# Kernel optimization log

Hardware: AMD Instinct MI355X
Metric: run time of the kernel (lower is better)

Reference implementation:

```python
import jax, jax.numpy as jnp
import numpy as np

B, T, C, H = 4, 4096, 1024, 64

def setup_inputs() -> dict:
    key = jax.random.key(0)
    k1, k2, k3, k4 = jax.random.split(key, 4)
    x = jax.random.normal(k1, (B, T, C), dtype=jnp.float32)
    # Linear(n_embed, head_size, bias=False), stored as [in, out] for x @ W
    s = 1.0 / np.sqrt(C)
    Wq = jax.random.uniform(k2, (C, H), dtype=jnp.float32, minval=-s, maxval=s)
    Wk = jax.random.uniform(k3, (C, H), dtype=jnp.float32, minval=-s, maxval=s)
    Wv = jax.random.uniform(k4, (C, H), dtype=jnp.float32, minval=-s, maxval=s)
    return {"x": x, "Wq": Wq, "Wk": Wk, "Wv": Wv}

def reference(x, Wq, Wk, Wv):
    Bn, Tn, Cn = x.shape
    q = x @ Wq  # [B,T,H]
    k = x @ Wk  # [B,T,H]
    v = x @ Wv  # [B,T,H]
    # NOTE: original scales by C**-0.5 (embedding dim), not head_size**-0.5
    wei = jnp.einsum('bqh,bkh->bqk', q, k) * (Cn ** -0.5)  # [B,T,T]
    causal = jnp.tril(jnp.ones((Tn, Tn), dtype=bool))
    wei = jnp.where(causal, wei, -jnp.inf)
    wei = jax.nn.softmax(wei, axis=-1)
    out = jnp.einsum('bqk,bkh->bqh', wei, v)  # [B,T,H]
    return out
```

## Files before the change

kernel.cpp:

```cpp
#include <hip/hip_runtime.h>
#include <hip/hip_bf16.h>


#define B_DIM 4
#define T_DIM 4096
#define C_DIM 1024
#define H_DIM 64
#define SCALE2 0.0450842066f
#define KP 72

typedef __attribute__((ext_vector_type(8))) short bf8;
typedef __attribute__((ext_vector_type(4))) short bf4;
typedef __attribute__((ext_vector_type(4))) float f32x4;
typedef __attribute__((ext_vector_type(16))) float f32x16;

__device__ __forceinline__ float fast_exp2(float f) {
    return __builtin_amdgcn_exp2f(f);
}
__device__ __forceinline__ ushort f2bf(float f) {
    union { float f; uint u; } x; x.f = f;
    const uint u = x.u;
    return (ushort)((u + 0x7FFFu + ((u >> 16) & 1u)) >> 16);
}
__device__ __forceinline__ uint cvt_pk_bf16(float lo, float hi) {
    uint r;
    asm("v_cvt_pk_bf16_f32 %0, %1, %2" : "=v"(r) : "v"(lo), "v"(hi));
    return r;
}
__device__ __forceinline__ void permswapf(float& a, float& b) {
    asm volatile("v_permlane32_swap_b32 %0, %1" : "+v"(a), "+v"(b));
}
__device__ __forceinline__ void permswapu(uint& a, uint& b) {
    asm volatile("v_permlane32_swap_b32 %0, %1" : "+v"(a), "+v"(b));
}
__device__ __forceinline__ bf8 frag_from(uint w0, uint w1, uint w2, uint w3) {
    union { uint u[4]; bf8 f; } x;
    x.u[0] = w0; x.u[1] = w1; x.u[2] = w2; x.u[3] = w3;
    return x.f;
}

__global__ __launch_bounds__(256) void wt_kernel(
    const float* __restrict__ Wq, const float* __restrict__ Wk,
    const float* __restrict__ Wv, ushort* __restrict__ wtg)
{
    const int id  = blockIdx.x * 256 + threadIdx.x;
    const int col = id >> 7;
    const int k8  = (id & 127) * 8;
    const int m   = col >> 6, lc = col & 63;
    const float* W = (m == 0) ? Wq : (m == 1) ? Wk : Wv;
    ushort o[8];
    #pragma unroll
    for (int i = 0; i < 8; ++i)
        o[i] = f2bf(W[(size_t)(k8 + i) * H_DIM + lc]);
    *(bf8*)&wtg[(size_t)col * C_DIM + k8] = *(bf8*)o;
}

__global__ __launch_bounds__(256) void qkv_mfma_kernel(
    const float* __restrict__ x, const ushort* __restrict__ wtg,
    ushort* __restrict__ qo, ushort* __restrict__ ko, ushort* __restrict__ vo)
{
    __shared__ ushort xs[32][KP];
    __shared__ ushort wts[192][KP];
    const int t    = threadIdx.x;
    const int lane = t & 63, wave = t >> 6;
    const int g    = lane >> 4, lid = lane & 15;
    const size_t r0 = (size_t)blockIdx.x * 32;

    f32x4 acc[2][3] = {};

    const int xrow = t >> 3, xcol = (t & 7) * 8;
    float4 xr[2];
    bf8 wreg[6];

    xr[0] = *(const float4*)&x[(r0 + xrow) * C_DIM + xcol];
    xr[1] = *(const float4*)&x[(r0 + xrow) * C_DIM + xcol + 4];
    #pragma unroll
    for (int it = 0; it < 6; ++it) {
        const int n = t + it * 256;
        wreg[it] = *(const bf8*)&wtg[(size_t)(n >> 3) * C_DIM + (n & 7) * 8];
    }

    for (int kc = 0; kc < C_DIM / 64; ++kc) {
        __syncthreads();
        {
            uint p[4];
            p[0] = cvt_pk_bf16(xr[0].x, xr[0].y); p[1] = cvt_pk_bf16(xr[0].z, xr[0].w);
            p[2] = cvt_pk_bf16(xr[1].x, xr[1].y); p[3] = cvt_pk_bf16(xr[1].z, xr[1].w);
            *(bf8*)&xs[xrow][xcol] = *(bf8*)p;
            #pragma unroll
            for (int it = 0; it < 6; ++it) {
                const int n = t + it * 256;
                *(bf8*)&wts[n >> 3][(n & 7) * 8] = wreg[it];
            }
        }
        __syncthreads();
        if (kc + 1 < C_DIM / 64) {
            const int kb = (kc + 1) * 64;
            xr[0] = *(const float4*)&x[(r0 + xrow) * C_DIM + kb + xcol];
            xr[1] = *(const float4*)&x[(r0 + xrow) * C_DIM + kb + xcol + 4];
            #pragma unroll
            for (int it = 0; it < 6; ++it) {
                const int n = t + it * 256;
                wreg[it] = *(const bf8*)&wtg[(size_t)(n >> 3) * C_DIM + kb + (n & 7) * 8];
            }
        }
        #pragma unroll
        for (int ks = 0; ks < 2; ++ks) {
            const bf8 a0 = *(const bf8*)&xs[lid][ks * 32 + g * 8];
            const bf8 a1 = *(const bf8*)&xs[16 + lid][ks * 32 + g * 8];
            #pragma unroll
            for (int j = 0; j < 3; ++j) {
                const int ct = wave * 3 + j;
                const bf8 bb = *(const bf8*)&wts[ct * 16 + lid][ks * 32 + g * 8];
                acc[0][j] = __builtin_amdgcn_mfma_f32_16x16x32_bf16(a0, bb, acc[0][j], 0, 0, 0);
                acc[1][j] = __builtin_amdgcn_mfma_f32_16x16x32_bf16(a1, bb, acc[1][j], 0, 0, 0);
            }
        }
    }

    #pragma unroll
    for (int rt = 0; rt < 2; ++rt)
        #pragma unroll
        for (int j = 0; j < 3; ++j) {
            const int ct = wave * 3 + j;
            const int m  = ct >> 2, lc = (ct & 3) * 16 + lid;
            ushort* dst = (m == 0) ? qo : (m == 1) ? ko : vo;
            const float sc = (m == 0) ? SCALE2 : 1.f;
            #pragma unroll
            for (int r = 0; r < 4; ++r) {
                const size_t row = r0 + rt * 16 + 4 * g + r;
                dst[row * H_DIM + lc] = f2bf(acc[rt][j][r] * sc);
            }
        }
}

__global__ __launch_bounds__(512) void flash_mfma_kernel(
    const ushort* __restrict__ q, const ushort* __restrict__ k,
    const ushort* __restrict__ v, float* __restrict__ pO,
    float* __restrict__ pl, float* __restrict__ out,
    int S, int nslots, int direct)
{
    const int qt  = 15 - blockIdx.y;
    const int c   = blockIdx.x;
    const int ntk = 4 * qt + 4;
    const int kt_begin = c * S;
    const int kt_end   = min((c + 1) * S, ntk);
    if (kt_begin >= kt_end) return;

    __shared__ ushort ks[64][KP];
    __shared__ ushort vt[64][KP];
    __shared__ float  lsh[8][32];

    const int t    = threadIdx.x;
    const int lane = t & 63, wave = t >> 6;
    const int l31  = lane & 31, hi = lane >> 5;
    const int b    = blockIdx.z;
    const int qrow0 = qt * 256 + wave * 32;
    const int ktw_max = (qrow0 + 31) >> 6;
    const size_t base = (size_t)b * T_DIM * H_DIM;

    bf8 qf[4];
    {
        const size_t qoff = base + (size_t)(qrow0 + l31) * H_DIM + hi * 8;
        #pragma unroll
        for (int kk = 0; kk < 4; ++kk)
            qf[kk] = *(const bf8*)&q[qoff + kk * 16];
    }

    f32x16 oa0 = {}, oa1 = {};
    float l_run = 0.f;

    const int krow = t >> 3, kc8 = (t & 7) * 8;
    const int vj = (t & 31) * 2, vc = (t >> 5) * 4;
    bf8 krg;
    bf4 vr0, vr1;
    {
        const int kg = kt_begin * 64;
        krg = *(const bf8*)&k[base + (size_t)(kg + krow) * H_DIM + kc8];
        vr0 = *(const bf4*)&v[base + (size_t)(kg + vj) * H_DIM + vc];
        vr1 = *(const bf4*)&v[base + (size_t)(kg + vj + 1) * H_DIM + vc];
    }

    #define BUILD_PA(dst, sv, bofs) do {                                   \
        uint a0_ = cvt_pk_bf16(sv[(bofs)+0], sv[(bofs)+1]);                \
        uint b0_ = cvt_pk_bf16(sv[(bofs)+4], sv[(bofs)+5]);                \
        uint a1_ = cvt_pk_bf16(sv[(bofs)+2], sv[(bofs)+3]);                \
        uint b1_ = cvt_pk_bf16(sv[(bofs)+6], sv[(bofs)+7]);                \
        permswapu(a0_, b0_); permswapu(a1_, b1_);                          \
        dst = frag_from(a0_, a1_, b0_, b1_);                               \
    } while (0)

    for (int kt64 = kt_begin; kt64 < kt_end; ++kt64) {
        __syncthreads();
        *(bf8*)&ks[krow][kc8] = krg;
        #pragma unroll
        for (int i = 0; i < 4; ++i) {
            const uint pk = (uint)(ushort)vr0[i] | ((uint)(ushort)vr1[i] << 16);
            *(uint*)&vt[vc + i][vj] = pk;
        }
        __syncthreads();
        if (kt64 + 1 < kt_end) {
            const int kg = (kt64 + 1) * 64;
            krg = *(const bf8*)&k[base + (size_t)(kg + krow) * H_DIM + kc8];
            vr0 = *(const bf4*)&v[base + (size_t)(kg + vj) * H_DIM + vc];
            vr1 = *(const bf4*)&v[base + (size_t)(kg + vj + 1) * H_DIM + vc];
        }
        if (kt64 > ktw_max) continue;

        f32x16 st0 = {}, st1 = {};
        #pragma unroll
        for (int kk = 0; kk < 4; ++kk) {
            const bf8 kfa = *(const bf8*)&ks[l31][kk * 16 + hi * 8];
            st0 = __builtin_amdgcn_mfma_f32_32x32x16_bf16(kfa, qf[kk], st0, 0, 0, 0);
        }
        #pragma unroll
        for (int kk = 0; kk < 4; ++kk) {
            const bf8 kfb = *(const bf8*)&ks[32 + l31][kk * 16 + hi * 8];
            st1 = __builtin_amdgcn_mfma_f32_32x32x16_bf16(kfb, qf[kk], st1, 0, 0, 0);
        }

        if (kt64 * 64 + 63 > qrow0) {
            const int qg  = qrow0 + l31;
            const int kb0 = kt64 * 64 + 4 * hi;
            #pragma unroll
            for (int r = 0; r < 16; ++r) {
                const int key0 = kb0 + (r & 3) + 8 * (r >> 2);
                if (key0 > qg)      st0[r] = -1e30f;
                if (key0 + 32 > qg) st1[r] = -1e30f;
            }
        }

        #pragma unroll
        for (int r = 0; r < 16; ++r) st0[r] = fast_exp2(st0[r]);
        #pragma unroll
        for (int r = 0; r < 16; ++r) st1[r] = fast_exp2(st1[r]);

        float sr[8];
        #pragma unroll
        for (int r = 0; r < 8; ++r)
            sr[r] = (st0[r] + st0[r + 8]) + (st1[r] + st1[r + 8]);
        #pragma unroll
        for (int off = 4; off > 0; off >>= 1)
            #pragma unroll
            for (int r = 0; r < 4; ++r)
                if (r < off) sr[r] += sr[r + off];
        float ls = sr[0];
        { float la = ls, lb = ls; permswapf(la, lb); ls = la + lb; }
        l_run += ls;

        bf8 pa[4];
        BUILD_PA(pa[0], st0, 0);
        BUILD_PA(pa[1], st0, 8);
        BUILD_PA(pa[2], st1, 0);
        BUILD_PA(pa[3], st1, 8);

        #pragma unroll
        for (int kk = 0; kk < 4; ++kk) {
            const bf8 vb0 = *(const bf8*)&vt[l31][kk * 16 + hi * 8];
            const bf8 vb1 = *(const bf8*)&vt[32 + l31][kk * 16 + hi * 8];
            oa0 = __builtin_amdgcn_mfma_f32_32x32x16_bf16(pa[kk], vb0, oa0, 0, 0, 0);
            oa1 = __builtin_amdgcn_mfma_f32_32x32x16_bf16(pa[kk], vb1, oa1, 0, 0, 0);
        }
    }
    #undef BUILD_PA

    if (direct) {
        if (lane < 32) lsh[wave][l31] = l_run;
        #pragma unroll
        for (int j = 0; j < 4; ++j) {
            const float4 lv = *(const float4*)&lsh[wave][8 * j + 4 * hi];
            const float iv[4] = {1.f / lv.x, 1.f / lv.y, 1.f / lv.z, 1.f / lv.w};
            #pragma unroll
            for (int rr = 0; rr < 4; ++rr) {
                const size_t rowoff = base + (size_t)(qrow0 + 8 * j + 4 * hi + rr) * H_DIM;
                out[rowoff + l31]      = oa0[4 * j + rr] * iv[rr];
                out[rowoff + 32 + l31] = oa1[4 * j + rr] * iv[rr];
            }
        }
    } else {
        const size_t u = ((size_t)b * 16 + qt) * nslots + c;
        float* po = pO + u * 16384;
        #pragma unroll
        for (int j = 0; j < 4; ++j)
            #pragma unroll
            for (int rr = 0; rr < 4; ++rr) {
                const int row = wave * 32 + 8 * j + 4 * hi + rr;
                po[(size_t)row * 64 + l31]      = oa0[4 * j + rr];
                po[(size_t)row * 64 + 32 + l31] = oa1[4 * j + rr];
            }
        if (lane < 32)
            pl[u * 256 + wave * 32 + l31] = l_run;
    }
}

__global__ __launch_bounds__(256) void combine_kernel(
    const float* __restrict__ pO, const float* __restrict__ pl,
    float* __restrict__ out, int S, int nslots)
{
    const int qt2 = blockIdx.x, b = blockIdx.y;
    const int qt = qt2 >> 1, half = qt2 & 1;
    const int ntk = 4 * qt + 4;
    const int nch = min(nslots, (ntk + S - 1) / S);
    const int t = threadIdx.x;
    const int row = half * 128 + (t >> 1), seg = (t & 1) * 32;
    const size_t u0 = ((size_t)b * 16 + qt) * nslots;

    float L = 0.f;
    float4 o[8] = {};
    for (int cc = 0; cc < nch; ++cc) {
        L += pl[(u0 + cc) * 256 + row];
        #pragma unroll
        for (int j = 0; j < 8; ++j) {
            const float4 p = *(const float4*)&pO[(u0 + cc) * 16384 +
                                                 (size_t)row * 64 + seg + j * 4];
            o[j].x += p.x; o[j].y += p.y;
            o[j].z += p.z; o[j].w += p.w;
        }
    }
    const float inv = 1.f / L;
    const size_t ob = (size_t)b * T_DIM * H_DIM + (size_t)(qt * 256 + row) * H_DIM + seg;
    #pragma unroll
    for (int j = 0; j < 8; ++j) {
        float4 r;
        r.x = o[j].x * inv; r.y = o[j].y * inv;
        r.z = o[j].z * inv; r.w = o[j].w * inv;
        *(float4*)&out[ob + j * 4] = r;
    }
}

extern "C" void kernel_launch(void* const* d_in, const int* in_sizes, int n_in,
                              void* d_out, int out_size, void* d_ws, size_t ws_size,
                              hipStream_t stream)
{
    const float* x  = (const float*)d_in[0];
    const float* Wq = (const float*)d_in[1];
    const float* Wk = (const float*)d_in[2];
    const float* Wv = (const float*)d_in[3];
    float* out = (float*)d_out;

    const size_t MB = 1u << 20;
    char* ws = (char*)d_ws;
    ushort* qb  = (ushort*)(ws);
    ushort* kb  = (ushort*)(ws + 2 * MB);
    ushort* vb  = (ushort*)(ws + 4 * MB);
    ushort* wtg = (ushort*)(ws + 6 * MB);
    float*  pO  = (float*)(ws + 7 * MB);

    int nslots, S;
    if      (ws_size >= 80 * MB) { nslots = 16; S = 4; }
    else if (ws_size >= 41 * MB) { nslots = 8;  S = 8; }
    else if (ws_size >= 24 * MB) { nslots = 4;  S = 16; }
    else                         { nslots = 1;  S = 64; }
    const int direct = (nslots == 1);
    float* pl = pO + (size_t)B_DIM * 16 * nslots * 16384;

    hipLaunchKernelGGL(wt_kernel, dim3(96), dim3(256), 0, stream, Wq, Wk, Wv, wtg);
    hipLaunchKernelGGL(qkv_mfma_kernel, dim3((B_DIM * T_DIM) / 32), dim3(256),
                       0, stream, x, wtg, qb, kb, vb);
    hipLaunchKernelGGL(flash_mfma_kernel, dim3(nslots, T_DIM / 256, B_DIM), dim3(512),
                       0, stream, qb, kb, vb, pO, pl, out, S, nslots, direct);
    if (!direct)
        hipLaunchKernelGGL(combine_kernel, dim3(32, B_DIM), dim3(256),
                           0, stream, pO, pl, out, S, nslots);
}
```

Measured before the change: 71.05 us.

## Store split-K partial outputs in bf16 and double the key-split count

Partial attention outputs are now written to the workspace as bf16 instead of fp32, and the combine kernel reads them with 16-byte vector loads and widens to fp32 before accumulating. The halved partial-buffer footprint is used to raise the number of key-range slots per query tile, giving more parallel blocks in the flash kernel with shorter chunks each. This cuts the traffic of the partial round-trip, but adds bf16 rounding to unnormalized partial sums and makes the combine loop over more slots.

```diff
diff --git a/kernel.cpp b/kernel.cpp
--- a/kernel.cpp
+++ b/kernel.cpp
@@ -21,6 +21,10 @@
     union { float f; uint u; } x; x.f = f;
     const uint u = x.u;
     return (ushort)((u + 0x7FFFu + ((u >> 16) & 1u)) >> 16);
+}
+__device__ __forceinline__ float bf2f(ushort h) {
+    union { uint u; float f; } x; x.u = ((uint)h) << 16;
+    return x.f;
 }
 __device__ __forceinline__ uint cvt_pk_bf16(float lo, float hi) {
     uint r;
@@ -136,7 +140,7 @@
 
 __global__ __launch_bounds__(512) void flash_mfma_kernel(
     const ushort* __restrict__ q, const ushort* __restrict__ k,
-    const ushort* __restrict__ v, float* __restrict__ pO,
+    const ushort* __restrict__ v, ushort* __restrict__ pO,
     float* __restrict__ pl, float* __restrict__ out,
     int S, int nslots, int direct)
 {
@@ -279,14 +283,14 @@
         }
     } else {
         const size_t u = ((size_t)b * 16 + qt) * nslots + c;
-        float* po = pO + u * 16384;
+        ushort* po = pO + u * 16384;
         #pragma unroll
         for (int j = 0; j < 4; ++j)
             #pragma unroll
             for (int rr = 0; rr < 4; ++rr) {
                 const int row = wave * 32 + 8 * j + 4 * hi + rr;
-                po[(size_t)row * 64 + l31]      = oa0[4 * j + rr];
-                po[(size_t)row * 64 + 32 + l31] = oa1[4 * j + rr];
+                po[(size_t)row * 64 + l31]      = f2bf(oa0[4 * j + rr]);
+                po[(size_t)row * 64 + 32 + l31] = f2bf(oa1[4 * j + rr]);
             }
         if (lane < 32)
             pl[u * 256 + wave * 32 + l31] = l_run;
@@ -294,7 +298,7 @@
 }
 
 __global__ __launch_bounds__(256) void combine_kernel(
-    const float* __restrict__ pO, const float* __restrict__ pl,
+    const ushort* __restrict__ pO, const float* __restrict__ pl,
     float* __restrict__ out, int S, int nslots)
 {
     const int qt2 = blockIdx.x, b = blockIdx.y;
@@ -306,25 +310,26 @@
     const size_t u0 = ((size_t)b * 16 + qt) * nslots;
 
     float L = 0.f;
-    float4 o[8] = {};
+    float oacc[32] = {};
     for (int cc = 0; cc < nch; ++cc) {
         L += pl[(u0 + cc) * 256 + row];
-        #pragma unroll
-        for (int j = 0; j < 8; ++j) {
-            const float4 p = *(const float4*)&pO[(u0 + cc) * 16384 +
-                                                 (size_t)row * 64 + seg + j * 4];
-            o[j].x += p.x; o[j].y += p.y;
-            o[j].z += p.z; o[j].w += p.w;
+        const ushort* pb = pO + (u0 + cc) * 16384 + (size_t)row * 64 + seg;
+        #pragma unroll
+        for (int jj = 0; jj < 4; ++jj) {
+            const bf8 pv = *(const bf8*)&pb[jj * 8];
+            #pragma unroll
+            for (int i = 0; i < 8; ++i)
+                oacc[jj * 8 + i] += bf2f((ushort)pv[i]);
         }
     }
     const float inv = 1.f / L;
     const size_t ob = (size_t)b * T_DIM * H_DIM + (size_t)(qt * 256 + row) * H_DIM + seg;
     #pragma unroll
-    for (int j = 0; j < 8; ++j) {
+    for (int jj = 0; jj < 8; ++jj) {
         float4 r;
-        r.x = o[j].x * inv; r.y = o[j].y * inv;
-        r.z = o[j].z * inv; r.w = o[j].w * inv;
-        *(float4*)&out[ob + j * 4] = r;
+        r.x = oacc[jj * 4 + 0] * inv; r.y = oacc[jj * 4 + 1] * inv;
+        r.z = oacc[jj * 4 + 2] * inv; r.w = oacc[jj * 4 + 3] * inv;
+        *(float4*)&out[ob + jj * 4] = r;
     }
 }
 
@@ -344,15 +349,16 @@
     ushort* kb  = (ushort*)(ws + 2 * MB);
     ushort* vb  = (ushort*)(ws + 4 * MB);
     ushort* wtg = (ushort*)(ws + 6 * MB);
-    float*  pO  = (float*)(ws + 7 * MB);
+    ushort* pO  = (ushort*)(ws + 7 * MB);
 
     int nslots, S;
-    if      (ws_size >= 80 * MB) { nslots = 16; S = 4; }
-    else if (ws_size >= 41 * MB) { nslots = 8;  S = 8; }
-    else if (ws_size >= 24 * MB) { nslots = 4;  S = 16; }
+    if      (ws_size >= 80 * MB) { nslots = 32; S = 2; }
+    else if (ws_size >= 48 * MB) { nslots = 16; S = 4; }
+    else if (ws_size >= 28 * MB) { nslots = 8;  S = 8; }
     else                         { nslots = 1;  S = 64; }
     const int direct = (nslots == 1);
-    float* pl = pO + (size_t)B_DIM * 16 * nslots * 16384;
+    float* pl = (float*)(ws + 7 * MB +
+                         (size_t)B_DIM * 16 * nslots * 16384 * sizeof(ushort));
 
     hipLaunchKernelGGL(wt_kernel, dim3(96), dim3(256), 0, stream, Wq, Wk, Wv, wtg);
     hipLaunchKernelGGL(qkv_mfma_kernel, dim3((B_DIM * T_DIM) / 32), dim3(256),
```

Result: slower. 83.32 us (+17.3%).

## Double-buffer K/V shared tiles with one barrier per iteration and MFMA priority

Applied to the files above, without the earlier changes.

Shared K and V tiles are double-buffered. The next tile's global loads are issued before compute and written to the alternate buffer after compute, which cuts the two barriers per iteration down to one. s_setprio is raised around the MFMA sections so those waves get scheduling priority. The workspace thresholds for choosing split counts are also raised. The trade-off is doubled LDS use, which may lower occupancy, and keeping prefetch registers live across the compute.

```diff
diff --git a/kernel.cpp b/kernel.cpp
--- a/kernel.cpp
+++ b/kernel.cpp
@@ -147,8 +147,8 @@
     const int kt_end   = min((c + 1) * S, ntk);
     if (kt_begin >= kt_end) return;
 
-    __shared__ ushort ks[64][KP];
-    __shared__ ushort vt[64][KP];
+    __shared__ ushort ks[2][64][KP];
+    __shared__ ushort vt[2][64][KP];
     __shared__ float  lsh[8][32];
 
     const int t    = threadIdx.x;
@@ -174,12 +174,22 @@
     const int vj = (t & 31) * 2, vc = (t >> 5) * 4;
     bf8 krg;
     bf4 vr0, vr1;
-    {
-        const int kg = kt_begin * 64;
-        krg = *(const bf8*)&k[base + (size_t)(kg + krow) * H_DIM + kc8];
-        vr0 = *(const bf4*)&v[base + (size_t)(kg + vj) * H_DIM + vc];
-        vr1 = *(const bf4*)&v[base + (size_t)(kg + vj + 1) * H_DIM + vc];
-    }
+
+    #define LOAD_STAGE(kt_) do {                                              \
+        const int kg_ = (kt_) * 64;                                           \
+        krg = *(const bf8*)&k[base + (size_t)(kg_ + krow) * H_DIM + kc8];     \
+        vr0 = *(const bf4*)&v[base + (size_t)(kg_ + vj) * H_DIM + vc];        \
+        vr1 = *(const bf4*)&v[base + (size_t)(kg_ + vj + 1) * H_DIM + vc];    \
+    } while (0)
+
+    #define WRITE_STAGE(buf_) do {                                            \
+        *(bf8*)&ks[buf_][krow][kc8] = krg;                                    \
+        _Pragma("unroll")                                                     \
+        for (int i = 0; i < 4; ++i) {                                         \
+            const uint pk = (uint)(ushort)vr0[i] | ((uint)(ushort)vr1[i] << 16); \
+            *(uint*)&vt[buf_][vc + i][vj] = pk;                               \
+        }                                                                     \
+    } while (0)
 
     #define BUILD_PA(dst, sv, bofs) do {                                   \
         uint a0_ = cvt_pk_bf16(sv[(bofs)+0], sv[(bofs)+1]);                \
@@ -190,79 +200,83 @@
         dst = frag_from(a0_, a1_, b0_, b1_);                               \
     } while (0)
 
+    LOAD_STAGE(kt_begin);
+    WRITE_STAGE(0);
+    __syncthreads();
+    int cur = 0;
+
     for (int kt64 = kt_begin; kt64 < kt_end; ++kt64) {
+        const bool more = (kt64 + 1 < kt_end);
+        if (more) LOAD_STAGE(kt64 + 1);
+
+        if (kt64 <= ktw_max) {
+            f32x16 st0 = {}, st1 = {};
+            __builtin_amdgcn_s_setprio(1);
+            #pragma unroll
+            for (int kk = 0; kk < 4; ++kk) {
+                const bf8 kfa = *(const bf8*)&ks[cur][l31][kk * 16 + hi * 8];
+                st0 = __builtin_amdgcn_mfma_f32_32x32x16_bf16(kfa, qf[kk], st0, 0, 0, 0);
+            }
+            #pragma unroll
+            for (int kk = 0; kk < 4; ++kk) {
+                const bf8 kfb = *(const bf8*)&ks[cur][32 + l31][kk * 16 + hi * 8];
+                st1 = __builtin_amdgcn_mfma_f32_32x32x16_bf16(kfb, qf[kk], st1, 0, 0, 0);
+            }
+            __builtin_amdgcn_s_setprio(0);
+
+            if (kt64 * 64 + 63 > qrow0) {
+                const int qg  = qrow0 + l31;
+                const int kb0 = kt64 * 64 + 4 * hi;
+                #pragma unroll
+                for (int r = 0; r < 16; ++r) {
+                    const int key0 = kb0 + (r & 3) + 8 * (r >> 2);
+                    if (key0 > qg)      st0[r] = -1e30f;
+                    if (key0 + 32 > qg) st1[r] = -1e30f;
+                }
+            }
+
+            #pragma unroll
+            for (int r = 0; r < 16; ++r) st0[r] = fast_exp2(st0[r]);
+            #pragma unroll
+            for (int r = 0; r < 16; ++r) st1[r] = fast_exp2(st1[r]);
+
+            float sr[8];
+            #pragma unroll
+            for (int r = 0; r < 8; ++r)
+                sr[r] = (st0[r] + st0[r + 8]) + (st1[r] + st1[r + 8]);
+            #pragma unroll
+            for (int off = 4; off > 0; off >>= 1)
+                #pragma unroll
+                for (int r = 0; r < 4; ++r)
+                    if (r < off) sr[r] += sr[r + off];
+            float ls = sr[0];
+            { float la = ls, lb = ls; permswapf(la, lb); ls = la + lb; }
+            l_run += ls;
+
+            bf8 pa[4];
+            BUILD_PA(pa[0], st0, 0);
+            BUILD_PA(pa[1], st0, 8);
+            BUILD_PA(pa[2], st1, 0);
+            BUILD_PA(pa[3], st1, 8);
+
+            __builtin_amdgcn_s_setprio(1);
+            #pragma unroll
+            for (int kk = 0; kk < 4; ++kk) {
+                const bf8 vb0 = *(const bf8*)&vt[cur][l31][kk * 16 + hi * 8];
+                const bf8 vb1 = *(const bf8*)&vt[cur][32 + l31][kk * 16 + hi * 8];
+                oa0 = __builtin_amdgcn_mfma_f32_32x32x16_bf16(pa[kk], vb0, oa0, 0, 0, 0);
+                oa1 = __builtin_amdgcn_mfma_f32_32x32x16_bf16(pa[kk], vb1, oa1, 0, 0, 0);
+            }
+            __builtin_amdgcn_s_setprio(0);
+        }
+
+        if (more) WRITE_STAGE(cur ^ 1);
         __syncthreads();
-        *(bf8*)&ks[krow][kc8] = krg;
-        #pragma unroll
-        for (int i = 0; i < 4; ++i) {
-            const uint pk = (uint)(ushort)vr0[i] | ((uint)(ushort)vr1[i] << 16);
-            *(uint*)&vt[vc + i][vj] = pk;
-        }
-        __syncthreads();
-        if (kt64 + 1 < kt_end) {
-            const int kg = (kt64 + 1) * 64;
-            krg = *(const bf8*)&k[base + (size_t)(kg + krow) * H_DIM + kc8];
-            vr0 = *(const bf4*)&v[base + (size_t)(kg + vj) * H_DIM + vc];
-            vr1 = *(const bf4*)&v[base + (size_t)(kg + vj + 1) * H_DIM + vc];
-        }
-        if (kt64 > ktw_max) continue;
-
-        f32x16 st0 = {}, st1 = {};
-        #pragma unroll
-        for (int kk = 0; kk < 4; ++kk) {
-            const bf8 kfa = *(const bf8*)&ks[l31][kk * 16 + hi * 8];
-            st0 = __builtin_amdgcn_mfma_f32_32x32x16_bf16(kfa, qf[kk], st0, 0, 0, 0);
-        }
-        #pragma unroll
-        for (int kk = 0; kk < 4; ++kk) {
-            const bf8 kfb = *(const bf8*)&ks[32 + l31][kk * 16 + hi * 8];
-            st1 = __builtin_amdgcn_mfma_f32_32x32x16_bf16(kfb, qf[kk], st1, 0, 0, 0);
-        }
-
-        if (kt64 * 64 + 63 > qrow0) {
-            const int qg  = qrow0 + l31;
-            const int kb0 = kt64 * 64 + 4 * hi;
-            #pragma unroll
-            for (int r = 0; r < 16; ++r) {
-                const int key0 = kb0 + (r & 3) + 8 * (r >> 2);
-                if (key0 > qg)      st0[r] = -1e30f;
-                if (key0 + 32 > qg) st1[r] = -1e30f;
-            }
-        }
-
-        #pragma unroll
-        for (int r = 0; r < 16; ++r) st0[r] = fast_exp2(st0[r]);
-        #pragma unroll
-        for (int r = 0; r < 16; ++r) st1[r] = fast_exp2(st1[r]);
-
-        float sr[8];
-        #pragma unroll
-        for (int r = 0; r < 8; ++r)
-            sr[r] = (st0[r] + st0[r + 8]) + (st1[r] + st1[r + 8]);
-        #pragma unroll
-        for (int off = 4; off > 0; off >>= 1)
-            #pragma unroll
-            for (int r = 0; r < 4; ++r)
-                if (r < off) sr[r] += sr[r + off];
-        float ls = sr[0];
-        { float la = ls, lb = ls; permswapf(la, lb); ls = la + lb; }
-        l_run += ls;
-
-        bf8 pa[4];
-        BUILD_PA(pa[0], st0, 0);
-        BUILD_PA(pa[1], st0, 8);
-        BUILD_PA(pa[2], st1, 0);
-        BUILD_PA(pa[3], st1, 8);
-
-        #pragma unroll
-        for (int kk = 0; kk < 4; ++kk) {
-            const bf8 vb0 = *(const bf8*)&vt[l31][kk * 16 + hi * 8];
-            const bf8 vb1 = *(const bf8*)&vt[32 + l31][kk * 16 + hi * 8];
-            oa0 = __builtin_amdgcn_mfma_f32_32x32x16_bf16(pa[kk], vb0, oa0, 0, 0, 0);
-            oa1 = __builtin_amdgcn_mfma_f32_32x32x16_bf16(pa[kk], vb1, oa1, 0, 0, 0);
-        }
+        cur ^= 1;
     }
     #undef BUILD_PA
+    #undef WRITE_STAGE
+    #undef LOAD_STAGE
 
     if (direct) {
         if (lane < 32) lsh[wave][l31] = l_run;
@@ -348,8 +362,8 @@
 
     int nslots, S;
     if      (ws_size >= 80 * MB) { nslots = 16; S = 4; }
-    else if (ws_size >= 41 * MB) { nslots = 8;  S = 8; }
-    else if (ws_size >= 24 * MB) { nslots = 4;  S = 16; }
+    else if (ws_size >= 48 * MB) { nslots = 8;  S = 8; }
+    else if (ws_size >= 28 * MB) { nslots = 4;  S = 16; }
     else                         { nslots = 1;  S = 64; }
     const int direct = (nslots == 1);
     float* pl = pO + (size_t)B_DIM * 16 * nslots * 16384;
```

After: 73.13 us. +2.9%, slower.
